# Kernel optimization log

Measured on AMD Instinct MI355X. Metric: run time of the kernel, lower is better.

## Reference

```python
import jax, jax.numpy as jnp
import numpy as np


def _lstm_layer(x, h0, c0, w_ih, w_hh, b):
    """x: [T,B,I], h0/c0: [B,H], w_ih: [4H,I], w_hh: [4H,H], b: [4H]. PyTorch gate order i,f,g,o."""
    H = h0.shape[-1]
    # Precompute input projection for all timesteps in one big GEMM.
    xg = jnp.einsum('tbi,gi->tbg', x, w_ih) + b  # [T,B,4H]

    def step(carry, xg_t):
        h, c = carry
        g = xg_t + h @ w_hh.T  # [B,4H]
        i, f, gg, o = jnp.split(g, 4, axis=-1)
        c_new = jax.nn.sigmoid(f) * c + jax.nn.sigmoid(i) * jnp.tanh(gg)
        h_new = jax.nn.sigmoid(o) * jnp.tanh(c_new)
        return (h_new, c_new), h_new

    (_, _), hs = jax.lax.scan(step, (h0, c0), xg)
    return hs  # [T,B,H]


def setup_inputs() -> dict:
    key = jax.random.key(0)
    ks = jax.random.split(key, 12)
    T, B, I, H, O, L = 2048, 32, 256, 512, 1024, 2
    s = 1.0 / np.sqrt(H)  # PyTorch LSTM init scale
    return {
        'x': jax.random.normal(ks[0], (T, B, I), jnp.float32),
        'h0': jnp.zeros((L, B, H), jnp.float32),
        'c0': jnp.zeros((L, B, H), jnp.float32),
        'w_ih0': jax.random.normal(ks[1], (4 * H, I), jnp.float32) * s,
        'w_hh0': jax.random.normal(ks[2], (4 * H, H), jnp.float32) * s,
        'b_ih0': jax.random.normal(ks[3], (4 * H,), jnp.float32) * s,
        'b_hh0': jax.random.normal(ks[4], (4 * H,), jnp.float32) * s,
        'w_ih1': jax.random.normal(ks[5], (4 * H, H), jnp.float32) * s,
        'w_hh1': jax.random.normal(ks[6], (4 * H, H), jnp.float32) * s,
        'b_ih1': jax.random.normal(ks[7], (4 * H,), jnp.float32) * s,
        'b_hh1': jax.random.normal(ks[8], (4 * H,), jnp.float32) * s,
        'fc_w': jax.random.normal(ks[9], (O, H), jnp.float32) * s,
        'fc_b': jax.random.normal(ks[10], (O,), jnp.float32) * s,
    }


def reference(x, h0, c0, w_ih0, w_hh0, b_ih0, b_hh0, w_ih1, w_hh1, b_ih1, b_hh1, fc_w, fc_b):
    h1 = _lstm_layer(x, h0[0], c0[0], w_ih0, w_hh0, b_ih0 + b_hh0)   # [T,B,H]
    h2 = _lstm_layer(h1, h0[1], c0[1], w_ih1, w_hh1, b_ih1 + b_hh1)  # [T,B,H]
    logits = h2[-1] @ fc_w.T + fc_b  # out[-1] -> fc, [B,O]
    return jax.nn.log_softmax(logits, axis=1)
```

## Files before the change

kernel.cpp:

```cpp
#include <hip/hip_runtime.h>
#include <stdint.h>

#define TT 2048
#define BB 32
#define II 256
#define HH 512
#define OO 1024
#define NWGL 64
#define NWG 128
#define RING 32
#define SLOTB (BB * HH * 2)

typedef __attribute__((ext_vector_type(8))) short short8;
typedef __attribute__((ext_vector_type(4))) float floatx4;

__device__ __forceinline__ unsigned short f2bf(float f) {
  union { float f; unsigned u; } v; v.f = f;
  unsigned r = v.u + 0x7FFFu + ((v.u >> 16) & 1u);
  return (unsigned short)(r >> 16);
}
__device__ __forceinline__ float bf2f(unsigned short b) {
  union { float f; unsigned u; } v; v.u = ((unsigned)b) << 16; return v.f;
}
__device__ __forceinline__ float sigmf(float x) { return 1.0f / (1.0f + __expf(-x)); }
__device__ __forceinline__ float tanhfast(float x) {
  float xc = fminf(fmaxf(x, -15.f), 15.f);
  float e = __expf(2.f * xc);
  return (e - 1.f) / (e + 1.f);
}

#define LD1(d, va, IMM)                                                     \
  asm volatile("global_load_dwordx4 %0, %1, off offset:" IMM " sc0 sc1"     \
               : "=v"(d) : "v"(va) : "memory")
#define LD1C(d, va, IMM)                                                    \
  asm volatile("global_load_dwordx4 %0, %1, off offset:" IMM                \
               : "=v"(d) : "v"(va) : "memory")

#define ISSUE8(dst, va) do {                                                \
    LD1(dst[0], va, "0");   LD1(dst[1], va, "64");                          \
    LD1(dst[2], va, "128"); LD1(dst[3], va, "192");                         \
    LD1(dst[4], va, "256"); LD1(dst[5], va, "320");                         \
    LD1(dst[6], va, "384"); LD1(dst[7], va, "448"); } while (0)
#define ISSUE8C(dst, va) do {                                               \
    LD1C(dst[0], va, "0");   LD1C(dst[1], va, "64");                        \
    LD1C(dst[2], va, "128"); LD1C(dst[3], va, "192");                       \
    LD1C(dst[4], va, "256"); LD1C(dst[5], va, "320");                       \
    LD1C(dst[6], va, "384"); LD1C(dst[7], va, "448"); } while (0)

#define WAITV(N) do {                                                       \
    asm volatile("s_waitcnt vmcnt(" #N ")" ::: "memory");                   \
    __builtin_amdgcn_sched_barrier(0); } while (0)

#define MF8(tt_, src, wbase) do {                                           \
    _Pragma("unroll")                                                       \
    for (int j = 0; j < 8; j++) {                                           \
      acc[0][tt_] = __builtin_amdgcn_mfma_f32_16x16x32_bf16(src[j], wf[0][(wbase) + j], acc[0][tt_], 0, 0, 0); \
      acc[1][tt_] = __builtin_amdgcn_mfma_f32_16x16x32_bf16(src[j], wf[1][(wbase) + j], acc[1][tt_], 0, 0, 0); \
    } } while (0)

#define PROGREAD(dst, addr64)                                               \
  asm volatile("global_load_dword %0, %1, off sc0 sc1"                      \
               : "=v"(dst) : "v"(addr64) : "memory")

#define SEQSTORE(arr, slot, val) do {                                       \
    if (lane == 0) {                                                        \
      unsigned long long _a = (unsigned long long)(arr) +                   \
          (unsigned long long)((slot) * 64 + g) * 4;                        \
      int _v = (val);                                                       \
      asm volatile("global_store_dword %0, %1, off sc0 sc1"                 \
                   :: "v"(_a), "v"(_v) : "memory");                         \
    } } while (0)

#define TAIL(hwaddr) do {                                                   \
  _Pragma("unroll")                                                         \
  for (int tau = 0; tau < 2; tau++) {                                       \
    _Pragma("unroll")                                                       \
    for (int tt = 0; tt < 2; tt++) {                                        \
      _Pragma("unroll")                                                     \
      for (int r = 0; r < 4; r++) {                                         \
        float val = acc[tau][tt][r];                                        \
        float nl = (gate == 2) ? tanhfast(val) : sigmf(val);                \
        int base2 = (lane & 48) | u;                                        \
        float iv = __shfl(nl, base2);                                       \
        float fv = __shfl(nl, base2 | 4);                                   \
        float gv = __shfl(nl, base2 | 8);                                   \
        float ov = __shfl(nl, base2 | 12);                                  \
        if (gate == 0) {                                                    \
          float cn = fv * cst[tau][tt][r] + iv * gv;                        \
          cst[tau][tt][r] = cn;                                             \
          float hn = ov * tanhfast(cn);                                     \
          int b = tt * 16 + krow * 4 + r;                                   \
          sh[b][tau * 4 + u] = f2bf(hn);                                    \
        }                                                                   \
      }                                                                     \
    }                                                                       \
  }                                                                         \
  asm volatile("s_waitcnt lgkmcnt(0)" ::: "memory");                        \
  __builtin_amdgcn_sched_barrier(0);                                        \
  if (lane < 32) {                                                          \
    short8 v = *reinterpret_cast<const short8*>(&sh[lane][0]);              \
    unsigned long long sa = (hwaddr) + stoff;                               \
    asm volatile("global_store_dwordx4 %0, %1, off sc0 sc1"                 \
                 :: "v"(sa), "v"(v) : "memory");                            \
  } } while (0)

__global__ void k_convert_x(const float* __restrict__ x, ushort* __restrict__ xb, int n4) {
  int i = blockIdx.x * blockDim.x + threadIdx.x;
  int stride = gridDim.x * blockDim.x;
  const float4* xf = reinterpret_cast<const float4*>(x);
  ushort4* ob = reinterpret_cast<ushort4*>(xb);
  for (; i < n4; i += stride) {
    float4 f = xf[i];
    ushort4 o;
    o.x = f2bf(f.x); o.y = f2bf(f.y); o.z = f2bf(f.z); o.w = f2bf(f.w);
    ob[i] = o;
  }
}

__global__ void k_init(const float* __restrict__ h0in,
                       ushort* __restrict__ h0ring, ushort* __restrict__ h1ring,
                       int* __restrict__ h0seq, int* __restrict__ h1seq,
                       int* __restrict__ pr1) {
  int i = threadIdx.x;
  ushort* s0 = h0ring + (RING - 1) * BB * HH;
  ushort* s1 = h1ring + (RING - 1) * BB * HH;
  for (int k = i; k < BB * HH; k += blockDim.x) {
    s0[k] = f2bf(h0in[k]);
    s1[k] = f2bf(h0in[BB * HH + k]);
  }
  for (int k = i; k < RING * 64; k += blockDim.x) {
    int v = (k >= (RING - 1) * 64) ? -1 : (int)0x80000000;
    h0seq[k] = v;
    h1seq[k] = v;
  }
  for (int k = i; k < 64; k += blockDim.x) pr1[k] = -1;
}

__global__ __launch_bounds__(64, 1) void k_lstm(
    const ushort* __restrict__ xb,
    const float* __restrict__ w_ih0, const float* __restrict__ w_hh0,
    const float* __restrict__ b_ih0, const float* __restrict__ b_hh0,
    const float* __restrict__ w_ih1, const float* __restrict__ w_hh1,
    const float* __restrict__ b_ih1, const float* __restrict__ b_hh1,
    const float* __restrict__ c0in,
    ushort* __restrict__ h0ring, ushort* __restrict__ h1ring,
    int* __restrict__ h0seq, int* __restrict__ h1seq,
    int* __restrict__ pr1)
{
  __shared__ ushort sh[BB][8];
  const int wg = blockIdx.x;
  const int lane = threadIdx.x;
  const bool isL0 = wg < NWGL;
  const int g = isL0 ? wg : wg - NWGL;
  const int col = lane & 15;
  const int krow = lane >> 4;
  const int u = col & 3;
  const int gate = col >> 2;

  short8 wf[2][32];
#define LOADW(dst, base, rowlen, kbase, tau) do {                             \
    const int _grow = gate * HH + g * 8 + (tau) * 4 + u;                      \
    const float* _p = (base) + (size_t)_grow * (rowlen) + (kbase) + krow * 8; \
    short8 _r;                                                                \
    _Pragma("unroll")                                                         \
    for (int _j = 0; _j < 8; _j++) _r[_j] = (short)f2bf(_p[_j]);              \
    (dst) = _r; } while (0)

  if (isL0) {
#pragma unroll
    for (int tau = 0; tau < 2; tau++) {
#pragma unroll
      for (int kk = 0; kk < 8; kk++)  LOADW(wf[tau][kk],      w_ih0, II, kk * 32, tau);
#pragma unroll
      for (int kk = 0; kk < 16; kk++) LOADW(wf[tau][8 + kk],  w_hh0, HH, kk * 32, tau);
    }
  } else {
#pragma unroll
    for (int tau = 0; tau < 2; tau++) {
#pragma unroll
      for (int kk = 0; kk < 16; kk++) LOADW(wf[tau][kk],      w_ih1, HH, kk * 32, tau);
#pragma unroll
      for (int kk = 0; kk < 16; kk++) LOADW(wf[tau][16 + kk], w_hh1, HH, kk * 32, tau);
    }
  }
  float bias[2];
#pragma unroll
  for (int tau = 0; tau < 2; tau++) {
    const int grow = gate * HH + g * 8 + tau * 4 + u;
    bias[tau] = isL0 ? (b_ih0[grow] + b_hh0[grow]) : (b_ih1[grow] + b_hh1[grow]);
  }

  float cst[2][2][4];
  {
    const float* cbase = c0in + (isL0 ? 0 : 1) * BB * HH;
#pragma unroll
    for (int tau = 0; tau < 2; tau++)
#pragma unroll
      for (int tt = 0; tt < 2; tt++)
#pragma unroll
        for (int r = 0; r < 4; r++) {
          int b = tt * 16 + krow * 4 + r;
          cst[tau][tt][r] = cbase[b * HH + g * 8 + tau * 4 + u];
        }
  }

  const unsigned long long h0rb = (unsigned long long)h0ring;
  const unsigned long long h1rb = (unsigned long long)h1ring;
  const int vo00 = col * 1024 + krow * 16;
  const unsigned long long stoff = (unsigned long long)(lane * 1024 + g * 16);

  short8 wa[8], wb[8], wc[8], wd[8];
  floatx4 acc[2][2];
  const floatx4 bi0 = (floatx4){ bias[0], bias[0], bias[0], bias[0] };
  const floatx4 bi1 = (floatx4){ bias[1], bias[1], bias[1], bias[1] };

  if (isL0) {
    const unsigned long long xbase = (unsigned long long)xb + (col * 512 + krow * 16);
    for (int t = 0; t < TT; ++t) {
      {
        const unsigned long long sa = (unsigned long long)h0seq +
            (unsigned long long)(((t + 31) & 31) * 64 + lane) * 4;
        int sv; PROGREAD(sv, sa); WAITV(0);
        while (!__all(sv == t - 1)) {
          __builtin_amdgcn_s_sleep(1); PROGREAD(sv, sa); WAITV(0);
        }
      }
      if (((t & 7) == 0) && t >= 32) {
        const unsigned long long pa = (unsigned long long)pr1 + lane * 4ull;
        int pv; PROGREAD(pv, pa); WAITV(0);
        while (!__all(pv >= t - 24)) {
          __builtin_amdgcn_s_sleep(4); PROGREAD(pv, pa); WAITV(0);
        }
      }
      acc[0][0] = bi0; acc[0][1] = bi0; acc[1][0] = bi1; acc[1][1] = bi1;
      const unsigned long long ha = h0rb + (unsigned long long)((t + 31) & 31) * SLOTB + vo00;
      const unsigned long long xa = xbase + (unsigned long long)t * (BB * II * 2);
      ISSUE8(wa, ha); ISSUE8(wb, ha + 512); ISSUE8(wc, ha + 16384); ISSUE8(wd, ha + 16896);
      WAITV(24); MF8(0, wa, 8);  ISSUE8C(wa, xa);
      WAITV(24); MF8(0, wb, 16); ISSUE8C(wb, xa + 8192);
      WAITV(24); MF8(1, wc, 8);
      WAITV(16); MF8(1, wd, 16);
      WAITV(8);  MF8(0, wa, 0);
      WAITV(0);  MF8(1, wb, 0);
      TAIL(h0rb + (unsigned long long)(t & 31) * SLOTB);
      WAITV(0);
      SEQSTORE(h0seq, (t & 31), t);
    }
  } else {
    for (int t = 0; t < TT; ++t) {
      {
        const unsigned long long sa0 = (unsigned long long)h0seq +
            (unsigned long long)((t & 31) * 64 + lane) * 4;
        const unsigned long long sa1 = (unsigned long long)h1seq +
            (unsigned long long)(((t + 31) & 31) * 64 + lane) * 4;
        int s0, s1; PROGREAD(s0, sa0); PROGREAD(s1, sa1); WAITV(0);
        while (!(__all(s0 == t) & __all(s1 == t - 1))) {
          __builtin_amdgcn_s_sleep(1);
          PROGREAD(s0, sa0); PROGREAD(s1, sa1); WAITV(0);
        }
      }
      acc[0][0] = bi0; acc[0][1] = bi0; acc[1][0] = bi1; acc[1][1] = bi1;
      const unsigned long long a0 = h0rb + (unsigned long long)(t & 31) * SLOTB + vo00;
      const unsigned long long a1 = h1rb + (unsigned long long)((t + 31) & 31) * SLOTB + vo00;
      ISSUE8(wa, a0); ISSUE8(wb, a0 + 512); ISSUE8(wc, a0 + 16384); ISSUE8(wd, a0 + 16896);
      WAITV(24); MF8(0, wa, 0); ISSUE8(wa, a1);
      WAITV(24); MF8(0, wb, 8); ISSUE8(wb, a1 + 512);
      WAITV(24); MF8(1, wc, 0); ISSUE8(wc, a1 + 16384);
      WAITV(24); MF8(1, wd, 8); ISSUE8(wd, a1 + 16896);
      WAITV(24); MF8(0, wa, 16);
      WAITV(16); MF8(0, wb, 24);
      WAITV(8);  MF8(1, wc, 16);
      WAITV(0);  MF8(1, wd, 24);
      if (lane == 0) {
        unsigned long long pa = (unsigned long long)pr1 + (unsigned long long)g * 4;
        int pv = t;
        asm volatile("global_store_dword %0, %1, off sc0 sc1"
                     :: "v"(pa), "v"(pv) : "memory");
      }
      TAIL(h1rb + (unsigned long long)(t & 31) * SLOTB);
      WAITV(0);
      SEQSTORE(h1seq, (t & 31), t);
    }
  }
}

__global__ __launch_bounds__(256) void k_fc(const ushort* __restrict__ h1,
                                            const float* __restrict__ fcw,
                                            const float* __restrict__ fcb,
                                            float* __restrict__ out) {
  __shared__ float hsh[HH];
  __shared__ float red[256];
  const int b = blockIdx.x, tid = threadIdx.x;
  for (int k = tid; k < HH; k += 256) hsh[k] = bf2f(h1[b * HH + k]);
  __syncthreads();
  float lg[4];
#pragma unroll
  for (int q = 0; q < 4; q++) {
    int o = q * 256 + tid;
    float acc = fcb[o];
    const float* wr = fcw + (size_t)o * HH;
#pragma unroll 4
    for (int k = 0; k < HH; k += 4) {
      float4 w4 = *reinterpret_cast<const float4*>(wr + k);
      acc += hsh[k] * w4.x + hsh[k + 1] * w4.y + hsh[k + 2] * w4.z + hsh[k + 3] * w4.w;
    }
    lg[q] = acc;
  }
  float m = fmaxf(fmaxf(lg[0], lg[1]), fmaxf(lg[2], lg[3]));
  red[tid] = m; __syncthreads();
  for (int s = 128; s > 0; s >>= 1) { if (tid < s) red[tid] = fmaxf(red[tid], red[tid + s]); __syncthreads(); }
  m = red[0]; __syncthreads();
  float se = 0.f;
#pragma unroll
  for (int q = 0; q < 4; q++) se += __expf(lg[q] - m);
  red[tid] = se; __syncthreads();
  for (int s = 128; s > 0; s >>= 1) { if (tid < s) red[tid] += red[tid + s]; __syncthreads(); }
  float lse = m + logf(red[0]);
#pragma unroll
  for (int q = 0; q < 4; q++) out[b * OO + q * 256 + tid] = lg[q] - lse;
}

extern "C" void kernel_launch(void* const* d_in, const int* in_sizes, int n_in,
                              void* d_out, int out_size, void* d_ws, size_t ws_size,
                              hipStream_t stream) {
  const float* x     = (const float*)d_in[0];
  const float* h0    = (const float*)d_in[1];
  const float* c0    = (const float*)d_in[2];
  const float* w_ih0 = (const float*)d_in[3];
  const float* w_hh0 = (const float*)d_in[4];
  const float* b_ih0 = (const float*)d_in[5];
  const float* b_hh0 = (const float*)d_in[6];
  const float* w_ih1 = (const float*)d_in[7];
  const float* w_hh1 = (const float*)d_in[8];
  const float* b_ih1 = (const float*)d_in[9];
  const float* b_hh1 = (const float*)d_in[10];
  const float* fcw   = (const float*)d_in[11];
  const float* fcb   = (const float*)d_in[12];
  float* out = (float*)d_out;

  char* ws = (char*)d_ws;
  size_t off = 0;
  ushort* xb     = (ushort*)(ws + off); off += (size_t)TT * BB * II * 2;
  ushort* h0ring = (ushort*)(ws + off); off += (size_t)RING * BB * HH * 2;
  ushort* h1ring = (ushort*)(ws + off); off += (size_t)RING * BB * HH * 2;
  int* h0seq = (int*)(ws + off); off += RING * 64 * sizeof(int);
  int* h1seq = (int*)(ws + off); off += RING * 64 * sizeof(int);
  int* pr1   = (int*)(ws + off); off += 64 * sizeof(int);

  k_convert_x<<<2048, 256, 0, stream>>>(x, xb, TT * BB * II / 4);
  k_init<<<1, 256, 0, stream>>>(h0, h0ring, h1ring, h0seq, h1seq, pr1);
  k_lstm<<<NWG, 64, 0, stream>>>(xb, w_ih0, w_hh0, b_ih0, b_hh0,
                                 w_ih1, w_hh1, b_ih1, b_hh1, c0,
                                 h0ring, h1ring, h0seq, h1seq, pr1);
  k_fc<<<BB, 256, 0, stream>>>(h1ring + (RING - 1) * BB * HH, fcw, fcb, out);
}
```

Before: 16.87 ms.

## Split K across four waves per workgroup with LDS reduction, fewer workgroups

Restructures the persistent LSTM kernel from 128 single-wave workgroups (8 hidden units each) to 32 four-wave workgroups, each owning 32 hidden units. The reduction dimension is split across the four waves, and partial gate sums are combined through LDS before the nonlinearity. Cross-workgroup flag polling now involves 16 producers per layer instead of 64, and the per-step pr1 progress array is replaced by a periodic check of h1seq. The aim is to cut global synchronisation fan-in and per-step latency, at the cost of an LDS reduction and two __syncthreads per step.

```diff
diff --git a/kernel.cpp b/kernel.cpp
--- a/kernel.cpp
+++ b/kernel.cpp
@@ -6,8 +6,8 @@
 #define II 256
 #define HH 512
 #define OO 1024
-#define NWGL 64
-#define NWG 128
+#define NWGL 16
+#define NWG 32
 #define RING 32
 #define SLOTB (BB * HH * 2)
 
@@ -41,68 +41,34 @@
     LD1(dst[2], va, "128"); LD1(dst[3], va, "192");                         \
     LD1(dst[4], va, "256"); LD1(dst[5], va, "320");                         \
     LD1(dst[6], va, "384"); LD1(dst[7], va, "448"); } while (0)
-#define ISSUE8C(dst, va) do {                                               \
-    LD1C(dst[0], va, "0");   LD1C(dst[1], va, "64");                        \
-    LD1C(dst[2], va, "128"); LD1C(dst[3], va, "192");                       \
-    LD1C(dst[4], va, "256"); LD1C(dst[5], va, "320");                       \
-    LD1C(dst[6], va, "384"); LD1C(dst[7], va, "448"); } while (0)
+#define ISSUE4(dst, va) do {                                                \
+    LD1(dst[0], va, "0");   LD1(dst[1], va, "64");                          \
+    LD1(dst[2], va, "128"); LD1(dst[3], va, "192"); } while (0)
+#define ISSUE2C(dst, va) do {                                               \
+    LD1C(dst[0], va, "0");  LD1C(dst[1], va, "64"); } while (0)
 
 #define WAITV(N) do {                                                       \
     asm volatile("s_waitcnt vmcnt(" #N ")" ::: "memory");                   \
     __builtin_amdgcn_sched_barrier(0); } while (0)
 
-#define MF8(tt_, src, wbase) do {                                           \
-    _Pragma("unroll")                                                       \
-    for (int j = 0; j < 8; j++) {                                           \
-      acc[0][tt_] = __builtin_amdgcn_mfma_f32_16x16x32_bf16(src[j], wf[0][(wbase) + j], acc[0][tt_], 0, 0, 0); \
-      acc[1][tt_] = __builtin_amdgcn_mfma_f32_16x16x32_bf16(src[j], wf[1][(wbase) + j], acc[1][tt_], 0, 0, 0); \
-    } } while (0)
-
 #define PROGREAD(dst, addr64)                                               \
   asm volatile("global_load_dword %0, %1, off sc0 sc1"                      \
                : "=v"(dst) : "v"(addr64) : "memory")
 
-#define SEQSTORE(arr, slot, val) do {                                       \
-    if (lane == 0) {                                                        \
-      unsigned long long _a = (unsigned long long)(arr) +                   \
-          (unsigned long long)((slot) * 64 + g) * 4;                        \
-      int _v = (val);                                                       \
-      asm volatile("global_store_dword %0, %1, off sc0 sc1"                 \
-                   :: "v"(_a), "v"(_v) : "memory");                         \
+#define VALIDATE(arr, slot, tag) do {                                       \
+    const unsigned long long _sa = (unsigned long long)(arr) +              \
+        (unsigned long long)((slot) * 16 + (lane & 15)) * 4;                \
+    int _sv; PROGREAD(_sv, _sa); WAITV(0);                                  \
+    while (!__all(_sv == (tag))) {                                          \
+      __builtin_amdgcn_s_sleep(1); PROGREAD(_sv, _sa); WAITV(0);            \
     } } while (0)
-
-#define TAIL(hwaddr) do {                                                   \
-  _Pragma("unroll")                                                         \
-  for (int tau = 0; tau < 2; tau++) {                                       \
-    _Pragma("unroll")                                                       \
-    for (int tt = 0; tt < 2; tt++) {                                        \
-      _Pragma("unroll")                                                     \
-      for (int r = 0; r < 4; r++) {                                         \
-        float val = acc[tau][tt][r];                                        \
-        float nl = (gate == 2) ? tanhfast(val) : sigmf(val);                \
-        int base2 = (lane & 48) | u;                                        \
-        float iv = __shfl(nl, base2);                                       \
-        float fv = __shfl(nl, base2 | 4);                                   \
-        float gv = __shfl(nl, base2 | 8);                                   \
-        float ov = __shfl(nl, base2 | 12);                                  \
-        if (gate == 0) {                                                    \
-          float cn = fv * cst[tau][tt][r] + iv * gv;                        \
-          cst[tau][tt][r] = cn;                                             \
-          float hn = ov * tanhfast(cn);                                     \
-          int b = tt * 16 + krow * 4 + r;                                   \
-          sh[b][tau * 4 + u] = f2bf(hn);                                    \
-        }                                                                   \
-      }                                                                     \
-    }                                                                       \
-  }                                                                         \
-  asm volatile("s_waitcnt lgkmcnt(0)" ::: "memory");                        \
-  __builtin_amdgcn_sched_barrier(0);                                        \
-  if (lane < 32) {                                                          \
-    short8 v = *reinterpret_cast<const short8*>(&sh[lane][0]);              \
-    unsigned long long sa = (hwaddr) + stoff;                               \
-    asm volatile("global_store_dwordx4 %0, %1, off sc0 sc1"                 \
-                 :: "v"(sa), "v"(v) : "memory");                            \
-  } } while (0)
+#define GUARDGE(arr, slot, tag) do {                                        \
+    const unsigned long long _sa = (unsigned long long)(arr) +              \
+        (unsigned long long)((slot) * 16 + (lane & 15)) * 4;                \
+    int _sv; PROGREAD(_sv, _sa); WAITV(0);                                  \
+    while (!__all(_sv >= (tag))) {                                          \
+      __builtin_amdgcn_s_sleep(4); PROGREAD(_sv, _sa); WAITV(0);            \
+    } } while (0)
 
 __global__ void k_convert_x(const float* __restrict__ x, ushort* __restrict__ xb, int n4) {
   int i = blockIdx.x * blockDim.x + threadIdx.x;
@@ -119,8 +85,7 @@
 
 __global__ void k_init(const float* __restrict__ h0in,
                        ushort* __restrict__ h0ring, ushort* __restrict__ h1ring,
-                       int* __restrict__ h0seq, int* __restrict__ h1seq,
-                       int* __restrict__ pr1) {
+                       int* __restrict__ h0seq, int* __restrict__ h1seq) {
   int i = threadIdx.x;
   ushort* s0 = h0ring + (RING - 1) * BB * HH;
   ushort* s1 = h1ring + (RING - 1) * BB * HH;
@@ -128,15 +93,14 @@
     s0[k] = f2bf(h0in[k]);
     s1[k] = f2bf(h0in[BB * HH + k]);
   }
-  for (int k = i; k < RING * 64; k += blockDim.x) {
-    int v = (k >= (RING - 1) * 64) ? -1 : (int)0x80000000;
+  for (int k = i; k < RING * 16; k += blockDim.x) {
+    int v = (k >= (RING - 1) * 16) ? -1 : (int)0x80000000;
     h0seq[k] = v;
     h1seq[k] = v;
   }
-  for (int k = i; k < 64; k += blockDim.x) pr1[k] = -1;
-}
-
-__global__ __launch_bounds__(64, 1) void k_lstm(
+}
+
+__global__ __launch_bounds__(256, 1) void k_lstm(
     const ushort* __restrict__ xb,
     const float* __restrict__ w_ih0, const float* __restrict__ w_hh0,
     const float* __restrict__ b_ih0, const float* __restrict__ b_hh0,
@@ -144,142 +108,217 @@
     const float* __restrict__ b_ih1, const float* __restrict__ b_hh1,
     const float* __restrict__ c0in,
     ushort* __restrict__ h0ring, ushort* __restrict__ h1ring,
-    int* __restrict__ h0seq, int* __restrict__ h1seq,
-    int* __restrict__ pr1)
+    int* __restrict__ h0seq, int* __restrict__ h1seq)
 {
-  __shared__ ushort sh[BB][8];
+  __shared__ floatx4 plds[4][3][2][2][64];
+  __shared__ ushort hsh[4][BB][8];
   const int wg = blockIdx.x;
-  const int lane = threadIdx.x;
+  const int tid = threadIdx.x;
+  const int w = tid >> 6;
+  const int lane = tid & 63;
   const bool isL0 = wg < NWGL;
-  const int g = isL0 ? wg : wg - NWGL;
+  const int G = isL0 ? wg : wg - NWGL;
   const int col = lane & 15;
   const int krow = lane >> 4;
   const int u = col & 3;
   const int gate = col >> 2;
 
-  short8 wf[2][32];
-#define LOADW(dst, base, rowlen, kbase, tau) do {                             \
-    const int _grow = gate * HH + g * 8 + (tau) * 4 + u;                      \
-    const float* _p = (base) + (size_t)_grow * (rowlen) + (kbase) + krow * 8; \
-    short8 _r;                                                                \
-    _Pragma("unroll")                                                         \
-    for (int _j = 0; _j < 8; _j++) _r[_j] = (short)f2bf(_p[_j]);              \
-    (dst) = _r; } while (0)
-
-  if (isL0) {
-#pragma unroll
-    for (int tau = 0; tau < 2; tau++) {
-#pragma unroll
-      for (int kk = 0; kk < 8; kk++)  LOADW(wf[tau][kk],      w_ih0, II, kk * 32, tau);
-#pragma unroll
-      for (int kk = 0; kk < 16; kk++) LOADW(wf[tau][8 + kk],  w_hh0, HH, kk * 32, tau);
-    }
-  } else {
-#pragma unroll
-    for (int tau = 0; tau < 2; tau++) {
-#pragma unroll
-      for (int kk = 0; kk < 16; kk++) LOADW(wf[tau][kk],      w_ih1, HH, kk * 32, tau);
-#pragma unroll
-      for (int kk = 0; kk < 16; kk++) LOADW(wf[tau][16 + kk], w_hh1, HH, kk * 32, tau);
-    }
-  }
-  float bias[2];
-#pragma unroll
-  for (int tau = 0; tau < 2; tau++) {
-    const int grow = gate * HH + g * 8 + tau * 4 + u;
-    bias[tau] = isL0 ? (b_ih0[grow] + b_hh0[grow]) : (b_ih1[grow] + b_hh1[grow]);
-  }
-
+  float biasv[2];
+#pragma unroll
+  for (int dt = 0; dt < 2; dt++) {
+    const int grow = gate * HH + G * 32 + (2 * w + dt) * 4 + u;
+    biasv[dt] = isL0 ? (b_ih0[grow] + b_hh0[grow]) : (b_ih1[grow] + b_hh1[grow]);
+  }
   float cst[2][2][4];
   {
     const float* cbase = c0in + (isL0 ? 0 : 1) * BB * HH;
 #pragma unroll
-    for (int tau = 0; tau < 2; tau++)
-#pragma unroll
-      for (int tt = 0; tt < 2; tt++)
+    for (int dt = 0; dt < 2; dt++)
+#pragma unroll
+      for (int bt = 0; bt < 2; bt++)
 #pragma unroll
         for (int r = 0; r < 4; r++) {
-          int b = tt * 16 + krow * 4 + r;
-          cst[tau][tt][r] = cbase[b * HH + g * 8 + tau * 4 + u];
+          int b = bt * 16 + krow * 4 + r;
+          cst[dt][bt][r] = cbase[b * HH + G * 32 + (2 * w + dt) * 4 + u];
         }
   }
 
   const unsigned long long h0rb = (unsigned long long)h0ring;
   const unsigned long long h1rb = (unsigned long long)h1ring;
   const int vo00 = col * 1024 + krow * 16;
-  const unsigned long long stoff = (unsigned long long)(lane * 1024 + g * 16);
-
-  short8 wa[8], wb[8], wc[8], wd[8];
-  floatx4 acc[2][2];
-  const floatx4 bi0 = (floatx4){ bias[0], bias[0], bias[0], bias[0] };
-  const floatx4 bi1 = (floatx4){ bias[1], bias[1], bias[1], bias[1] };
+  const unsigned long long stoff =
+      (unsigned long long)(lane * 1024 + (G * 4 + w) * 16);
+
+#define FINISH_PUBLISH(seqarr, ringbase, slot, tag) do {                    \
+    _Pragma("unroll")                                                       \
+    for (int f = 0; f < 4; f++) {                                           \
+      if (f != w) {                                                         \
+        int sidx = (w > f) ? (w - 1) : w;                                   \
+        _Pragma("unroll")                                                   \
+        for (int dt = 0; dt < 2; dt++)                                      \
+          _Pragma("unroll")                                                 \
+          for (int bt = 0; bt < 2; bt++)                                    \
+            plds[f][sidx][dt][bt][lane] = acc[2 * f + dt][bt];              \
+      }                                                                     \
+    }                                                                       \
+    __syncthreads();                                                        \
+    floatx4 accf[2][2];                                                     \
+    _Pragma("unroll")                                                       \
+    for (int dt = 0; dt < 2; dt++)                                          \
+      _Pragma("unroll")                                                     \
+      for (int bt = 0; bt < 2; bt++) {                                      \
+        floatx4 s = acc[2 * w + dt][bt];                                    \
+        s = s + plds[w][0][dt][bt][lane];                                   \
+        s = s + plds[w][1][dt][bt][lane];                                   \
+        s = s + plds[w][2][dt][bt][lane];                                   \
+        float bsc = biasv[dt];                                              \
+        s[0] += bsc; s[1] += bsc; s[2] += bsc; s[3] += bsc;                 \
+        accf[dt][bt] = s;                                                   \
+      }                                                                     \
+    _Pragma("unroll")                                                       \
+    for (int dt = 0; dt < 2; dt++)                                          \
+      _Pragma("unroll")                                                     \
+      for (int bt = 0; bt < 2; bt++)                                        \
+        _Pragma("unroll")                                                   \
+        for (int r = 0; r < 4; r++) {                                       \
+          float val = accf[dt][bt][r];                                      \
+          float nl = (gate == 2) ? tanhfast(val) : sigmf(val);              \
+          int base2 = (lane & 48) | u;                                      \
+          float iv = __shfl(nl, base2);                                     \
+          float fv = __shfl(nl, base2 | 4);                                 \
+          float gv = __shfl(nl, base2 | 8);                                 \
+          float ov = __shfl(nl, base2 | 12);                                \
+          if (gate == 0) {                                                  \
+            float cn = fv * cst[dt][bt][r] + iv * gv;                       \
+            cst[dt][bt][r] = cn;                                            \
+            float hn = ov * tanhfast(cn);                                   \
+            int b = bt * 16 + krow * 4 + r;                                 \
+            hsh[w][b][dt * 4 + u] = f2bf(hn);                               \
+          }                                                                 \
+        }                                                                   \
+    asm volatile("s_waitcnt lgkmcnt(0)" ::: "memory");                      \
+    __builtin_amdgcn_sched_barrier(0);                                      \
+    if (lane < 32) {                                                        \
+      short8 v = *reinterpret_cast<const short8*>(&hsh[w][lane][0]);        \
+      unsigned long long sa = (ringbase) +                                  \
+          (unsigned long long)(slot) * SLOTB + stoff;                       \
+      asm volatile("global_store_dwordx4 %0, %1, off sc0 sc1"               \
+                   :: "v"(sa), "v"(v) : "memory");                          \
+    }                                                                       \
+    WAITV(0);                                                               \
+    __syncthreads();                                                        \
+    if (tid == 0) {                                                         \
+      unsigned long long _pa = (unsigned long long)(seqarr) +               \
+          (unsigned long long)((slot) * 16 + G) * 4;                        \
+      int _pv = (tag);                                                      \
+      asm volatile("global_store_dword %0, %1, off sc0 sc1"                 \
+                   :: "v"(_pa), "v"(_pv) : "memory");                       \
+    } } while (0)
 
   if (isL0) {
-    const unsigned long long xbase = (unsigned long long)xb + (col * 512 + krow * 16);
+    short8 wfx[8][2], wfh[8][4];
+#pragma unroll
+    for (int tau = 0; tau < 8; tau++) {
+      const int grow = gate * HH + G * 32 + tau * 4 + u;
+#pragma unroll
+      for (int j = 0; j < 2; j++) {
+        const float* p = w_ih0 + (size_t)grow * II + (2 * w + j) * 32 + krow * 8;
+        short8 rr;
+#pragma unroll
+        for (int q = 0; q < 8; q++) rr[q] = (short)f2bf(p[q]);
+        wfx[tau][j] = rr;
+      }
+#pragma unroll
+      for (int j = 0; j < 4; j++) {
+        const float* p = w_hh0 + (size_t)grow * HH + (4 * w + j) * 32 + krow * 8;
+        short8 rr;
+#pragma unroll
+        for (int q = 0; q < 8; q++) rr[q] = (short)f2bf(p[q]);
+        wfh[tau][j] = rr;
+      }
+    }
+    const unsigned long long xbase =
+        (unsigned long long)xb + (col * 512 + krow * 16 + w * 128);
     for (int t = 0; t < TT; ++t) {
-      {
-        const unsigned long long sa = (unsigned long long)h0seq +
-            (unsigned long long)(((t + 31) & 31) * 64 + lane) * 4;
-        int sv; PROGREAD(sv, sa); WAITV(0);
-        while (!__all(sv == t - 1)) {
-          __builtin_amdgcn_s_sleep(1); PROGREAD(sv, sa); WAITV(0);
-        }
-      }
-      if (((t & 7) == 0) && t >= 32) {
-        const unsigned long long pa = (unsigned long long)pr1 + lane * 4ull;
-        int pv; PROGREAD(pv, pa); WAITV(0);
-        while (!__all(pv >= t - 24)) {
-          __builtin_amdgcn_s_sleep(4); PROGREAD(pv, pa); WAITV(0);
-        }
-      }
-      acc[0][0] = bi0; acc[0][1] = bi0; acc[1][0] = bi1; acc[1][1] = bi1;
-      const unsigned long long ha = h0rb + (unsigned long long)((t + 31) & 31) * SLOTB + vo00;
+      VALIDATE(h0seq, (t + 31) & 31, t - 1);
+      if (((t & 7) == 0) && t >= 32) GUARDGE(h1seq, (t - 24) & 31, t - 24);
+      floatx4 acc[8][2];
+#pragma unroll
+      for (int tau = 0; tau < 8; tau++) {
+        acc[tau][0] = (floatx4){0.f, 0.f, 0.f, 0.f};
+        acc[tau][1] = (floatx4){0.f, 0.f, 0.f, 0.f};
+      }
       const unsigned long long xa = xbase + (unsigned long long)t * (BB * II * 2);
-      ISSUE8(wa, ha); ISSUE8(wb, ha + 512); ISSUE8(wc, ha + 16384); ISSUE8(wd, ha + 16896);
-      WAITV(24); MF8(0, wa, 8);  ISSUE8C(wa, xa);
-      WAITV(24); MF8(0, wb, 16); ISSUE8C(wb, xa + 8192);
-      WAITV(24); MF8(1, wc, 8);
-      WAITV(16); MF8(1, wd, 16);
-      WAITV(8);  MF8(0, wa, 0);
-      WAITV(0);  MF8(1, wb, 0);
-      TAIL(h0rb + (unsigned long long)(t & 31) * SLOTB);
+      const unsigned long long ha =
+          h0rb + (unsigned long long)((t + 31) & 31) * SLOTB + vo00 + w * 256;
+      short8 sx0[2], sh0[4], sx1[2], sh1[4];
+      ISSUE2C(sx0, xa); ISSUE4(sh0, ha);
+      ISSUE2C(sx1, xa + 8192); ISSUE4(sh1, ha + 16384);
+      WAITV(6);
+#pragma unroll
+      for (int tau = 0; tau < 8; tau++) {
+#pragma unroll
+        for (int j = 0; j < 2; j++)
+          acc[tau][0] = __builtin_amdgcn_mfma_f32_16x16x32_bf16(sx0[j], wfx[tau][j], acc[tau][0], 0, 0, 0);
+#pragma unroll
+        for (int j = 0; j < 4; j++)
+          acc[tau][0] = __builtin_amdgcn_mfma_f32_16x16x32_bf16(sh0[j], wfh[tau][j], acc[tau][0], 0, 0, 0);
+      }
       WAITV(0);
-      SEQSTORE(h0seq, (t & 31), t);
+#pragma unroll
+      for (int tau = 0; tau < 8; tau++) {
+#pragma unroll
+        for (int j = 0; j < 2; j++)
+          acc[tau][1] = __builtin_amdgcn_mfma_f32_16x16x32_bf16(sx1[j], wfx[tau][j], acc[tau][1], 0, 0, 0);
+#pragma unroll
+        for (int j = 0; j < 4; j++)
+          acc[tau][1] = __builtin_amdgcn_mfma_f32_16x16x32_bf16(sh1[j], wfh[tau][j], acc[tau][1], 0, 0, 0);
+      }
+      FINISH_PUBLISH(h0seq, h0rb, (t & 31), t);
     }
   } else {
+    short8 wf[8][8];
+#pragma unroll
+    for (int tau = 0; tau < 8; tau++) {
+      const int grow = gate * HH + G * 32 + tau * 4 + u;
+      const float* wbase = (w < 2) ? w_ih1 : w_hh1;
+#pragma unroll
+      for (int j = 0; j < 8; j++) {
+        const float* p = wbase + (size_t)grow * HH + ((w & 1) * 8 + j) * 32 + krow * 8;
+        short8 rr;
+#pragma unroll
+        for (int q = 0; q < 8; q++) rr[q] = (short)f2bf(p[q]);
+        wf[tau][j] = rr;
+      }
+    }
     for (int t = 0; t < TT; ++t) {
-      {
-        const unsigned long long sa0 = (unsigned long long)h0seq +
-            (unsigned long long)((t & 31) * 64 + lane) * 4;
-        const unsigned long long sa1 = (unsigned long long)h1seq +
-            (unsigned long long)(((t + 31) & 31) * 64 + lane) * 4;
-        int s0, s1; PROGREAD(s0, sa0); PROGREAD(s1, sa1); WAITV(0);
-        while (!(__all(s0 == t) & __all(s1 == t - 1))) {
-          __builtin_amdgcn_s_sleep(1);
-          PROGREAD(s0, sa0); PROGREAD(s1, sa1); WAITV(0);
-        }
-      }
-      acc[0][0] = bi0; acc[0][1] = bi0; acc[1][0] = bi1; acc[1][1] = bi1;
-      const unsigned long long a0 = h0rb + (unsigned long long)(t & 31) * SLOTB + vo00;
-      const unsigned long long a1 = h1rb + (unsigned long long)((t + 31) & 31) * SLOTB + vo00;
-      ISSUE8(wa, a0); ISSUE8(wb, a0 + 512); ISSUE8(wc, a0 + 16384); ISSUE8(wd, a0 + 16896);
-      WAITV(24); MF8(0, wa, 0); ISSUE8(wa, a1);
-      WAITV(24); MF8(0, wb, 8); ISSUE8(wb, a1 + 512);
-      WAITV(24); MF8(1, wc, 0); ISSUE8(wc, a1 + 16384);
-      WAITV(24); MF8(1, wd, 8); ISSUE8(wd, a1 + 16896);
-      WAITV(24); MF8(0, wa, 16);
-      WAITV(16); MF8(0, wb, 24);
-      WAITV(8);  MF8(1, wc, 16);
-      WAITV(0);  MF8(1, wd, 24);
-      if (lane == 0) {
-        unsigned long long pa = (unsigned long long)pr1 + (unsigned long long)g * 4;
-        int pv = t;
-        asm volatile("global_store_dword %0, %1, off sc0 sc1"
-                     :: "v"(pa), "v"(pv) : "memory");
-      }
-      TAIL(h1rb + (unsigned long long)(t & 31) * SLOTB);
+      VALIDATE(h0seq, (t & 31), t);
+      VALIDATE(h1seq, (t + 31) & 31, t - 1);
+      floatx4 acc[8][2];
+#pragma unroll
+      for (int tau = 0; tau < 8; tau++) {
+        acc[tau][0] = (floatx4){0.f, 0.f, 0.f, 0.f};
+        acc[tau][1] = (floatx4){0.f, 0.f, 0.f, 0.f};
+      }
+      const unsigned long long va =
+          ((w < 2) ? (h0rb + (unsigned long long)(t & 31) * SLOTB)
+                   : (h1rb + (unsigned long long)((t + 31) & 31) * SLOTB)) +
+          vo00 + (w & 1) * 512;
+      short8 wa[8], wb[8];
+      ISSUE8(wa, va); ISSUE8(wb, va + 16384);
+      WAITV(8);
+#pragma unroll
+      for (int tau = 0; tau < 8; tau++)
+#pragma unroll
+        for (int j = 0; j < 8; j++)
+          acc[tau][0] = __builtin_amdgcn_mfma_f32_16x16x32_bf16(wa[j], wf[tau][j], acc[tau][0], 0, 0, 0);
       WAITV(0);
-      SEQSTORE(h1seq, (t & 31), t);
+#pragma unroll
+      for (int tau = 0; tau < 8; tau++)
+#pragma unroll
+        for (int j = 0; j < 8; j++)
+          acc[tau][1] = __builtin_amdgcn_mfma_f32_16x16x32_bf16(wb[j], wf[tau][j], acc[tau][1], 0, 0, 0);
+      FINISH_PUBLISH(h1seq, h1rb, (t & 31), t);
     }
   }
 }
@@ -288,10 +327,10 @@
                                             const float* __restrict__ fcw,
                                             const float* __restrict__ fcb,
                                             float* __restrict__ out) {
-  __shared__ float hsh[HH];
+  __shared__ float hsh2[HH];
   __shared__ float red[256];
   const int b = blockIdx.x, tid = threadIdx.x;
-  for (int k = tid; k < HH; k += 256) hsh[k] = bf2f(h1[b * HH + k]);
+  for (int k = tid; k < HH; k += 256) hsh2[k] = bf2f(h1[b * HH + k]);
   __syncthreads();
   float lg[4];
 #pragma unroll
@@ -302,7 +341,7 @@
 #pragma unroll 4
     for (int k = 0; k < HH; k += 4) {
       float4 w4 = *reinterpret_cast<const float4*>(wr + k);
-      acc += hsh[k] * w4.x + hsh[k + 1] * w4.y + hsh[k + 2] * w4.z + hsh[k + 3] * w4.w;
+      acc += hsh2[k] * w4.x + hsh2[k + 1] * w4.y + hsh2[k + 2] * w4.z + hsh2[k + 3] * w4.w;
     }
     lg[q] = acc;
   }
@@ -343,14 +382,13 @@
   ushort* xb     = (ushort*)(ws + off); off += (size_t)TT * BB * II * 2;
   ushort* h0ring = (ushort*)(ws + off); off += (size_t)RING * BB * HH * 2;
   ushort* h1ring = (ushort*)(ws + off); off += (size_t)RING * BB * HH * 2;
-  int* h0seq = (int*)(ws + off); off += RING * 64 * sizeof(int);
-  int* h1seq = (int*)(ws + off); off += RING * 64 * sizeof(int);
-  int* pr1   = (int*)(ws + off); off += 64 * sizeof(int);
+  int* h0seq = (int*)(ws + off); off += RING * 16 * sizeof(int);
+  int* h1seq = (int*)(ws + off); off += RING * 16 * sizeof(int);
 
   k_convert_x<<<2048, 256, 0, stream>>>(x, xb, TT * BB * II / 4);
-  k_init<<<1, 256, 0, stream>>>(h0, h0ring, h1ring, h0seq, h1seq, pr1);
-  k_lstm<<<NWG, 64, 0, stream>>>(xb, w_ih0, w_hh0, b_ih0, b_hh0,
-                                 w_ih1, w_hh1, b_ih1, b_hh1, c0,
-                                 h0ring, h1ring, h0seq, h1seq, pr1);
+  k_init<<<1, 256, 0, stream>>>(h0, h0ring, h1ring, h0seq, h1seq);
+  k_lstm<<<NWG, 256, 0, stream>>>(xb, w_ih0, w_hh0, b_ih0, b_hh0,
+                                  w_ih1, w_hh1, b_ih1, b_hh1, c0,
+                                  h0ring, h1ring, h0seq, h1seq);
   k_fc<<<BB, 256, 0, stream>>>(h1ring + (RING - 1) * BB * HH, fcw, fcb, out);
 }
```

Result: slower. 17.31 ms (+2.6%).

## Replicate sequence flags and stagger h-load order to cut polling contention

Applied to the files above, without the earlier changes.

Sequence flags are now written to NREP replicas, and each workgroup polls its own replica instead of all 128 workgroups polling one cache line. The separate pr1 progress array is dropped. The layer-0 ring-overwrite guard now reads the layer-1 h1seq flags instead. Each workgroup also rotates the order in which it loads the four h-vector chunks, spreading simultaneous reads across addresses. Sleep intervals in the spin loops grow. Writers pay eight flag stores per step, which adds latency to the critical-path signal, and the larger sleeps may delay wakeup.

```diff
diff --git a/kernel.cpp b/kernel.cpp
--- a/kernel.cpp
+++ b/kernel.cpp
@@ -9,7 +9,9 @@
 #define NWGL 64
 #define NWG 128
 #define RING 32
+#define NREP 8
 #define SLOTB (BB * HH * 2)
+#define SEQN (NREP * RING * 64)
 
 typedef __attribute__((ext_vector_type(8))) short short8;
 typedef __attribute__((ext_vector_type(4))) float floatx4;
@@ -64,11 +66,29 @@
 
 #define SEQSTORE(arr, slot, val) do {                                       \
     if (lane == 0) {                                                        \
-      unsigned long long _a = (unsigned long long)(arr) +                   \
-          (unsigned long long)((slot) * 64 + g) * 4;                        \
-      int _v = (val);                                                       \
-      asm volatile("global_store_dword %0, %1, off sc0 sc1"                 \
-                   :: "v"(_a), "v"(_v) : "memory");                         \
+      _Pragma("unroll")                                                     \
+      for (int _r = 0; _r < NREP; _r++) {                                   \
+        unsigned long long _a = (unsigned long long)(arr) +                 \
+            (unsigned long long)(_r * RING * 64 + (slot) * 64 + g) * 4;     \
+        int _v = (val);                                                     \
+        asm volatile("global_store_dword %0, %1, off sc0 sc1"               \
+                     :: "v"(_a), "v"(_v) : "memory");                       \
+      }                                                                     \
+    } } while (0)
+
+#define VALIDATE(arr, slot, tag) do {                                       \
+    const unsigned long long _sa = (unsigned long long)(arr) +              \
+        (unsigned long long)(repoff + (slot) * 64 + lane) * 4;              \
+    int _sv; PROGREAD(_sv, _sa); WAITV(0);                                  \
+    while (!__all(_sv == (tag))) {                                          \
+      __builtin_amdgcn_s_sleep(2); PROGREAD(_sv, _sa); WAITV(0);            \
+    } } while (0)
+#define GUARDGE(arr, slot, tag) do {                                        \
+    const unsigned long long _sa = (unsigned long long)(arr) +              \
+        (unsigned long long)(repoff + (slot) * 64 + lane) * 4;              \
+    int _sv; PROGREAD(_sv, _sa); WAITV(0);                                  \
+    while (!__all(_sv >= (tag))) {                                          \
+      __builtin_amdgcn_s_sleep(4); PROGREAD(_sv, _sa); WAITV(0);            \
     } } while (0)
 
 #define TAIL(hwaddr) do {                                                   \
@@ -104,6 +124,27 @@
                  :: "v"(sa), "v"(v) : "memory");                            \
   } } while (0)
 
+#define L0BODY(A0,W0,T0, A1,W1,T1, A2,W2,T2, A3,W3,T3) do {                 \
+    ISSUE8(wa, A0); ISSUE8(wb, A1); ISSUE8(wc, A2); ISSUE8(wd, A3);         \
+    WAITV(24); MF8(T0, wa, W0); ISSUE8C(wa, xa);                            \
+    WAITV(24); MF8(T1, wb, W1); ISSUE8C(wb, xa + 8192);                     \
+    WAITV(24); MF8(T2, wc, W2);                                             \
+    WAITV(16); MF8(T3, wd, W3);                                             \
+    WAITV(8);  MF8(0, wa, 0);                                               \
+    WAITV(0);  MF8(1, wb, 0); } while (0)
+
+#define L1BODY(A0,W0,T0, A1,W1,T1, A2,W2,T2, A3,W3,T3,                      \
+               A4,W4,T4, A5,W5,T5, A6,W6,T6, A7,W7,T7) do {                 \
+    ISSUE8(wa, A0); ISSUE8(wb, A1); ISSUE8(wc, A2); ISSUE8(wd, A3);         \
+    WAITV(24); MF8(T0, wa, W0); ISSUE8(wa, A4);                             \
+    WAITV(24); MF8(T1, wb, W1); ISSUE8(wb, A5);                             \
+    WAITV(24); MF8(T2, wc, W2); ISSUE8(wc, A6);                             \
+    WAITV(24); MF8(T3, wd, W3); ISSUE8(wd, A7);                             \
+    WAITV(24); MF8(T4, wa, W4);                                             \
+    WAITV(16); MF8(T5, wb, W5);                                             \
+    WAITV(8);  MF8(T6, wc, W6);                                             \
+    WAITV(0);  MF8(T7, wd, W7); } while (0)
+
 __global__ void k_convert_x(const float* __restrict__ x, ushort* __restrict__ xb, int n4) {
   int i = blockIdx.x * blockDim.x + threadIdx.x;
   int stride = gridDim.x * blockDim.x;
@@ -119,8 +160,7 @@
 
 __global__ void k_init(const float* __restrict__ h0in,
                        ushort* __restrict__ h0ring, ushort* __restrict__ h1ring,
-                       int* __restrict__ h0seq, int* __restrict__ h1seq,
-                       int* __restrict__ pr1) {
+                       int* __restrict__ h0seq, int* __restrict__ h1seq) {
   int i = threadIdx.x;
   ushort* s0 = h0ring + (RING - 1) * BB * HH;
   ushort* s1 = h1ring + (RING - 1) * BB * HH;
@@ -128,12 +168,12 @@
     s0[k] = f2bf(h0in[k]);
     s1[k] = f2bf(h0in[BB * HH + k]);
   }
-  for (int k = i; k < RING * 64; k += blockDim.x) {
-    int v = (k >= (RING - 1) * 64) ? -1 : (int)0x80000000;
+  for (int k = i; k < SEQN; k += blockDim.x) {
+    int slot = (k % (RING * 64)) / 64;
+    int v = (slot == RING - 1) ? -1 : (int)0x80000000;
     h0seq[k] = v;
     h1seq[k] = v;
   }
-  for (int k = i; k < 64; k += blockDim.x) pr1[k] = -1;
 }
 
 __global__ __launch_bounds__(64, 1) void k_lstm(
@@ -144,8 +184,7 @@
     const float* __restrict__ b_ih1, const float* __restrict__ b_hh1,
     const float* __restrict__ c0in,
     ushort* __restrict__ h0ring, ushort* __restrict__ h1ring,
-    int* __restrict__ h0seq, int* __restrict__ h1seq,
-    int* __restrict__ pr1)
+    int* __restrict__ h0seq, int* __restrict__ h1seq)
 {
   __shared__ ushort sh[BB][8];
   const int wg = blockIdx.x;
@@ -156,6 +195,8 @@
   const int krow = lane >> 4;
   const int u = col & 3;
   const int gate = col >> 2;
+  const int repoff = (g & (NREP - 1)) * RING * 64;
+  const int rot = g & 3;
 
   short8 wf[2][32];
 #define LOADW(dst, base, rowlen, kbase, tau) do {                             \
@@ -217,31 +258,17 @@
   if (isL0) {
     const unsigned long long xbase = (unsigned long long)xb + (col * 512 + krow * 16);
     for (int t = 0; t < TT; ++t) {
-      {
-        const unsigned long long sa = (unsigned long long)h0seq +
-            (unsigned long long)(((t + 31) & 31) * 64 + lane) * 4;
-        int sv; PROGREAD(sv, sa); WAITV(0);
-        while (!__all(sv == t - 1)) {
-          __builtin_amdgcn_s_sleep(1); PROGREAD(sv, sa); WAITV(0);
-        }
-      }
-      if (((t & 7) == 0) && t >= 32) {
-        const unsigned long long pa = (unsigned long long)pr1 + lane * 4ull;
-        int pv; PROGREAD(pv, pa); WAITV(0);
-        while (!__all(pv >= t - 24)) {
-          __builtin_amdgcn_s_sleep(4); PROGREAD(pv, pa); WAITV(0);
-        }
-      }
+      VALIDATE(h0seq, (t + 31) & 31, t - 1);
+      if (((t & 7) == 0) && t >= 32) GUARDGE(h1seq, (t - 24) & 31, t - 24);
       acc[0][0] = bi0; acc[0][1] = bi0; acc[1][0] = bi1; acc[1][1] = bi1;
       const unsigned long long ha = h0rb + (unsigned long long)((t + 31) & 31) * SLOTB + vo00;
       const unsigned long long xa = xbase + (unsigned long long)t * (BB * II * 2);
-      ISSUE8(wa, ha); ISSUE8(wb, ha + 512); ISSUE8(wc, ha + 16384); ISSUE8(wd, ha + 16896);
-      WAITV(24); MF8(0, wa, 8);  ISSUE8C(wa, xa);
-      WAITV(24); MF8(0, wb, 16); ISSUE8C(wb, xa + 8192);
-      WAITV(24); MF8(1, wc, 8);
-      WAITV(16); MF8(1, wd, 16);
-      WAITV(8);  MF8(0, wa, 0);
-      WAITV(0);  MF8(1, wb, 0);
+      switch (rot) {
+        case 0:  L0BODY(ha,8,0,        ha+512,16,0,   ha+16384,8,1,  ha+16896,16,1); break;
+        case 1:  L0BODY(ha+512,16,0,   ha+16384,8,1,  ha+16896,16,1, ha,8,0);        break;
+        case 2:  L0BODY(ha+16384,8,1,  ha+16896,16,1, ha,8,0,        ha+512,16,0);   break;
+        default: L0BODY(ha+16896,16,1, ha,8,0,        ha+512,16,0,   ha+16384,8,1);  break;
+      }
       TAIL(h0rb + (unsigned long long)(t & 31) * SLOTB);
       WAITV(0);
       SEQSTORE(h0seq, (t & 31), t);
@@ -250,32 +277,35 @@
     for (int t = 0; t < TT; ++t) {
       {
         const unsigned long long sa0 = (unsigned long long)h0seq +
-            (unsigned long long)((t & 31) * 64 + lane) * 4;
+            (unsigned long long)(repoff + (t & 31) * 64 + lane) * 4;
         const unsigned long long sa1 = (unsigned long long)h1seq +
-            (unsigned long long)(((t + 31) & 31) * 64 + lane) * 4;
+            (unsigned long long)(repoff + ((t + 31) & 31) * 64 + lane) * 4;
         int s0, s1; PROGREAD(s0, sa0); PROGREAD(s1, sa1); WAITV(0);
         while (!(__all(s0 == t) & __all(s1 == t - 1))) {
-          __builtin_amdgcn_s_sleep(1);
+          __builtin_amdgcn_s_sleep(2);
           PROGREAD(s0, sa0); PROGREAD(s1, sa1); WAITV(0);
         }
       }
       acc[0][0] = bi0; acc[0][1] = bi0; acc[1][0] = bi1; acc[1][1] = bi1;
       const unsigned long long a0 = h0rb + (unsigned long long)(t & 31) * SLOTB + vo00;
       const unsigned long long a1 = h1rb + (unsigned long long)((t + 31) & 31) * SLOTB + vo00;
-      ISSUE8(wa, a0); ISSUE8(wb, a0 + 512); ISSUE8(wc, a0 + 16384); ISSUE8(wd, a0 + 16896);
-      WAITV(24); MF8(0, wa, 0); ISSUE8(wa, a1);
-      WAITV(24); MF8(0, wb, 8); ISSUE8(wb, a1 + 512);
-      WAITV(24); MF8(1, wc, 0); ISSUE8(wc, a1 + 16384);
-      WAITV(24); MF8(1, wd, 8); ISSUE8(wd, a1 + 16896);
-      WAITV(24); MF8(0, wa, 16);
-      WAITV(16); MF8(0, wb, 24);
-      WAITV(8);  MF8(1, wc, 16);
-      WAITV(0);  MF8(1, wd, 24);
-      if (lane == 0) {
-        unsigned long long pa = (unsigned long long)pr1 + (unsigned long long)g * 4;
-        int pv = t;
-        asm volatile("global_store_dword %0, %1, off sc0 sc1"
-                     :: "v"(pa), "v"(pv) : "memory");
+      switch (rot) {
+        case 0:
+          L1BODY(a0,0,0,       a0+512,8,0,    a0+16384,0,1,  a0+16896,8,1,
+                 a1,16,0,      a1+512,24,0,   a1+16384,16,1, a1+16896,24,1);
+          break;
+        case 1:
+          L1BODY(a0+16384,0,1, a0+16896,8,1,  a1,16,0,       a1+512,24,0,
+                 a1+16384,16,1,a1+16896,24,1, a0,0,0,        a0+512,8,0);
+          break;
+        case 2:
+          L1BODY(a1,16,0,      a1+512,24,0,   a1+16384,16,1, a1+16896,24,1,
+                 a0,0,0,       a0+512,8,0,    a0+16384,0,1,  a0+16896,8,1);
+          break;
+        default:
+          L1BODY(a1+16384,16,1,a1+16896,24,1, a0,0,0,        a0+512,8,0,
+                 a0+16384,0,1, a0+16896,8,1,  a1,16,0,       a1+512,24,0);
+          break;
       }
       TAIL(h1rb + (unsigned long long)(t & 31) * SLOTB);
       WAITV(0);
@@ -343,14 +373,13 @@
   ushort* xb     = (ushort*)(ws + off); off += (size_t)TT * BB * II * 2;
   ushort* h0ring = (ushort*)(ws + off); off += (size_t)RING * BB * HH * 2;
   ushort* h1ring = (ushort*)(ws + off); off += (size_t)RING * BB * HH * 2;
-  int* h0seq = (int*)(ws + off); off += RING * 64 * sizeof(int);
-  int* h1seq = (int*)(ws + off); off += RING * 64 * sizeof(int);
-  int* pr1   = (int*)(ws + off); off += 64 * sizeof(int);
+  int* h0seq = (int*)(ws + off); off += SEQN * sizeof(int);
+  int* h1seq = (int*)(ws + off); off += SEQN * sizeof(int);
 
   k_convert_x<<<2048, 256, 0, stream>>>(x, xb, TT * BB * II / 4);
-  k_init<<<1, 256, 0, stream>>>(h0, h0ring, h1ring, h0seq, h1seq, pr1);
+  k_init<<<1, 256, 0, stream>>>(h0, h0ring, h1ring, h0seq, h1seq);
   k_lstm<<<NWG, 64, 0, stream>>>(xb, w_ih0, w_hh0, b_ih0, b_hh0,
                                  w_ih1, w_hh1, b_ih1, b_hh1, c0,
-                                 h0ring, h1ring, h0seq, h1seq, pr1);
+                                 h0ring, h1ring, h0seq, h1seq);
   k_fc<<<BB, 256, 0, stream>>>(h1ring + (RING - 1) * BB * HH, fcw, fcb, out);
 }
```

Result: slower. 18.02 ms (+6.8%).
